# Kernel optimization log

Hardware: AMD Instinct MI355X
Metric: run time of the kernel (lower is better)

Reference implementation:

```python
import jax, jax.numpy as jnp
import numpy as np

B, L, C, V = 16, 600, 256, 256
OUT_SEQ = 6000
KSZ = 5
DILATIONS = (1, 2, 4)
N_BLOCKS = 10
COND = 256  # speaker(128) + noise(128)
TEMP = 10.0
EPS = 1e-5


def _ccbn(x, cond, gw, gb, bw, bb):
    # x: (B, C, L); conditional batch-norm: per-channel stats over (batch, length),
    # gamma/beta predicted from condition vector.
    mu = jnp.mean(x, axis=(0, 2), keepdims=True)
    var = jnp.var(x, axis=(0, 2), keepdims=True)
    xn = (x - mu) * jax.lax.rsqrt(var + EPS)
    gamma = 1.0 + cond @ gw + gb  # (B, C)
    beta = cond @ bw + bb         # (B, C)
    return xn * gamma[:, :, None] + beta[:, :, None]


def _conv1d(x, w, b, dil=1):
    # x: (B, C_in, L); w: (C_out, C_in, K)
    y = jax.lax.conv_general_dilated(
        x, w, window_strides=(1,), padding='SAME', rhs_dilation=(dil,),
        dimension_numbers=('NCH', 'OIH', 'NCH'))
    return y + b[None, :, None]


def setup_inputs() -> dict:
    key = jax.random.key(0)
    ks = jax.random.split(key, 20)
    s = 0.02
    inp = {
        'inputs': jax.random.randint(ks[0], (B, L), 0, V),
        'speaker_embeddings': jax.random.normal(ks[1], (B, 128), jnp.float32),
        'noise': jax.random.normal(ks[2], (B, 128), jnp.float32),
        'emb': jax.random.normal(ks[3], (V, C), jnp.float32) * s,
        # 10 blocks x 3 dilated convs
        'conv_w': jax.random.normal(ks[4], (N_BLOCKS, 3, C, C, KSZ), jnp.float32) * s,
        'conv_b': jnp.zeros((N_BLOCKS, 3, C), jnp.float32),
        # CCBN projections per conv (gamma/beta from condition)
        'g_w': jax.random.normal(ks[5], (N_BLOCKS, 3, COND, C), jnp.float32) * s,
        'g_b': jnp.zeros((N_BLOCKS, 3, C), jnp.float32),
        'b_w': jax.random.normal(ks[6], (N_BLOCKS, 3, COND, C), jnp.float32) * s,
        'b_b': jnp.zeros((N_BLOCKS, 3, C), jnp.float32),
        # TokenLength head: 2 CCBNs + conv1 (256->256,k1) + conv2 (256->1,k1)
        'tl_g_w': jax.random.normal(ks[7], (2, COND, C), jnp.float32) * s,
        'tl_g_b': jnp.zeros((2, C), jnp.float32),
        'tl_b_w': jax.random.normal(ks[8], (2, COND, C), jnp.float32) * s,
        'tl_b_b': jnp.zeros((2, C), jnp.float32),
        'tl_conv1_w': jax.random.normal(ks[9], (C, C, 1), jnp.float32) * s,
        'tl_conv1_b': jnp.zeros((C,), jnp.float32),
        'tl_conv2_w': jax.random.normal(ks[10], (1, C, 1), jnp.float32) * s,
        'tl_conv2_b': jnp.zeros((1,), jnp.float32),
    }
    return inp


def reference(inputs, speaker_embeddings, noise, emb, conv_w, conv_b,
              g_w, g_b, b_w, b_b, tl_g_w, tl_g_b, tl_b_w, tl_b_b,
              tl_conv1_w, tl_conv1_b, tl_conv2_w, tl_conv2_b):
    cond = jnp.concatenate([speaker_embeddings, noise], axis=-1)  # (B, COND)
    x = emb[inputs]                    # (B, L, C)
    x = jnp.transpose(x, (0, 2, 1))    # (B, C, L)

    # 10 unaligned blocks: residual stacks of CCBN -> ReLU -> dilated conv
    for blk in range(N_BLOCKS):
        y = x
        for j, d in enumerate(DILATIONS):
            y = jax.nn.relu(_ccbn(y, cond, g_w[blk, j], g_b[blk, j], b_w[blk, j], b_b[blk, j]))
            y = _conv1d(y, conv_w[blk, j], conv_b[blk, j], dil=d)
        x = x + y
    unaligned = x  # (B, C, L)

    # TokenLength head
    t = jax.nn.relu(_ccbn(unaligned, cond, tl_g_w[0], tl_g_b[0], tl_b_w[0], tl_b_b[0]))
    t = _conv1d(t, tl_conv1_w, tl_conv1_b)
    t = jax.nn.relu(_ccbn(t, cond, tl_g_w[1], tl_g_b[1], tl_b_w[1], tl_b_b[1]))
    t = _conv1d(t, tl_conv2_w, tl_conv2_b)  # (B, 1, L)
    token_lengths = jax.nn.relu(t[:, 0, :])  # (B, L)

    token_ends = jnp.cumsum(token_lengths, axis=-1)        # (B, L)
    token_centers = token_ends - token_lengths / 2.0        # (B, L)
    aligned_lengths = token_ends

    out_pos = jnp.arange(OUT_SEQ, dtype=jnp.float32)         # (OUT,)
    diff = token_centers[:, None, :] - out_pos[None, :, None]  # (B, OUT, L)
    logits = -(diff * diff) / TEMP
    weights = jax.nn.softmax(logits, axis=-1)                # (B, OUT, L)

    feats = jnp.transpose(unaligned, (0, 2, 1))              # (B, L, C)
    aligned_features = jnp.einsum('bol,blc->boc', weights, feats)  # (B, OUT, C)
    return aligned_features, aligned_lengths
```

## Files before the change

kernel.cpp:

```cpp
#include <hip/hip_runtime.h>
#include <math.h>
#include <stdint.h>

#define EPSv 1e-5f

typedef short short8 __attribute__((ext_vector_type(8)));
typedef float floatx4 __attribute__((ext_vector_type(4)));

__device__ __forceinline__ unsigned short f2bf(float x) {
  unsigned u = __float_as_uint(x);
  unsigned r = (u + 0x7fffu + ((u >> 16) & 1u)) >> 16;
  return (unsigned short)r;
}

__device__ __forceinline__ void gld_lds16(const void* g, void* l) {
  __builtin_amdgcn_global_load_lds(
      (const __attribute__((address_space(1))) unsigned*)(uintptr_t)g,
      (__attribute__((address_space(3))) unsigned*)(uintptr_t)l,
      16, 0, 0);
}

__global__ void k_zero(float* __restrict__ p) {
  p[blockIdx.x * 256 + threadIdx.x] = 0.f;
}

__global__ void k_gamma_beta(const float* __restrict__ spk, const float* __restrict__ noise,
                             const float* __restrict__ g_w, const float* __restrict__ g_b,
                             const float* __restrict__ b_w, const float* __restrict__ b_b,
                             const float* __restrict__ tl_g_w, const float* __restrict__ tl_g_b,
                             const float* __restrict__ tl_b_w, const float* __restrict__ tl_b_b,
                             float* __restrict__ gammas, float* __restrict__ betas) {
  __shared__ float condl[16*256];
  int t = threadIdx.x;
  for (int idx = t; idx < 4096; idx += 256) {
    int b = idx >> 8, k = idx & 255;
    condl[idx] = (k < 128) ? spk[b*128 + k] : noise[b*128 + k - 128];
  }
  __syncthreads();
  int i = blockIdx.x;
  const float *gw, *bw, *gbias, *bbias;
  if (i < 30) { gw = g_w + (size_t)i*65536; bw = b_w + (size_t)i*65536; gbias = g_b + i*256; bbias = b_b + i*256; }
  else { int j = i - 30; gw = tl_g_w + (size_t)j*65536; bw = tl_b_w + (size_t)j*65536; gbias = tl_g_b + j*256; bbias = tl_b_b + j*256; }
  int co = (t & 63) + blockIdx.y * 64;
  int slot = t >> 6;
  float g[4] = {0.f,0.f,0.f,0.f}, bt[4] = {0.f,0.f,0.f,0.f};
  for (int k = 0; k < 256; ++k) {
    float gwv = gw[k*256 + co];
    float bwv = bw[k*256 + co];
    #pragma unroll
    for (int bb = 0; bb < 4; ++bb) {
      float cv = condl[(slot*4 + bb)*256 + k];
      g[bb]  = fmaf(cv, gwv, g[bb]);
      bt[bb] = fmaf(cv, bwv, bt[bb]);
    }
  }
  #pragma unroll
  for (int bb = 0; bb < 4; ++bb) {
    int b = slot*4 + bb;
    gammas[i*4096 + b*256 + co] = 1.0f + g[bb] + gbias[co];
    betas [i*4096 + b*256 + co] = bt[bb] + bbias[co];
  }
}

template<int TAPS>
__device__ __forceinline__ void wprep_body(const float* __restrict__ src,
                                           unsigned short* __restrict__ dst,
                                           int cotile, int chunk, int t) {
  int cow = t >> 2, ci8 = (t & 3) * 8;
  const float* s0 = src + ((size_t)(cotile*64 + cow)*256 + chunk*32 + ci8)*TAPS;
  float v[8*TAPS];
  #pragma unroll
  for (int i = 0; i < 8*TAPS; ++i) v[i] = s0[i];
  unsigned short* dblk = dst + (size_t)cotile*(8*TAPS*4096) + (size_t)chunk*(TAPS*4096);
  #pragma unroll
  for (int tap = 0; tap < TAPS; ++tap) {
    unsigned hi2[4], lo2[4];
    #pragma unroll
    for (int jj = 0; jj < 4; ++jj) {
      float a = v[(jj*2+0)*TAPS + tap], b = v[(jj*2+1)*TAPS + tap];
      unsigned short ha = f2bf(a), hb = f2bf(b);
      unsigned short la = f2bf(a - __uint_as_float((unsigned)ha << 16));
      unsigned short lb = f2bf(b - __uint_as_float((unsigned)hb << 16));
      hi2[jj] = (unsigned)ha | ((unsigned)hb << 16);
      lo2[jj] = (unsigned)la | ((unsigned)lb << 16);
    }
    uint4 H; H.x = hi2[0]; H.y = hi2[1]; H.z = hi2[2]; H.w = hi2[3];
    uint4 L; L.x = lo2[0]; L.y = lo2[1]; L.z = lo2[2]; L.w = lo2[3];
    *(uint4*)(dblk + (size_t)(tap*2)*2048 + cow*32 + ci8) = H;
    *(uint4*)(dblk + (size_t)(tap*2+1)*2048 + cow*32 + ci8) = L;
  }
}

__global__ __launch_bounds__(256) void k_wprep(const float* __restrict__ conv_w,
                                               const float* __restrict__ tl_c1_w,
                                               unsigned short* __restrict__ wp) {
  int cc = blockIdx.x;
  int cotile = blockIdx.y >> 3, chunk = blockIdx.y & 7;
  if (cc == 30) wprep_body<1>(tl_c1_w, wp + (size_t)30*655360, cotile, chunk, threadIdx.x);
  else          wprep_body<5>(conv_w + (size_t)cc*327680, wp + (size_t)cc*655360, cotile, chunk, threadIdx.x);
}

__global__ void k_embed2(const int* __restrict__ inp, const float* __restrict__ emb,
                         float* __restrict__ x, float* __restrict__ stat0) {
  int bx = blockIdx.x;
  int c = threadIdx.x;
  int r0 = bx * 60;
  float s = 0.f, s2 = 0.f;
  for (int r = 0; r < 60; ++r) {
    int row = inp[r0 + r];
    float v = emb[(size_t)row*256 + c];
    x[(size_t)(r0 + r)*256 + c] = v;
    s += v; s2 = fmaf(v, v, s2);
  }
  atomicAdd(&stat0[c], s);
  atomicAdd(&stat0[256 + c], s2);
}

__global__ __launch_bounds__(256) void k_norm(const float* __restrict__ z,
                      const float* __restrict__ stat,
                      const float* __restrict__ gam, const float* __restrict__ bet,
                      unsigned short* __restrict__ zn) {
  __shared__ float s_sc[32];
  __shared__ float s_sh[32];
  int b = blockIdx.x, chunk = blockIdx.y, rg = blockIdx.z;
  int t = threadIdx.x;
  if (t < 32) {
    int c = chunk*32 + t;
    float s = stat[c], s2 = stat[256 + c];
    float mu = s * (1.0f/9600.0f);
    float var = s2 * (1.0f/9600.0f) - mu*mu;
    float rs = rsqrtf(var + EPSv);
    float scale = rs * gam[b*256 + c];
    s_sc[t] = scale;
    s_sh[t] = fmaf(-mu, scale, bet[b*256 + c]);
  }
  __syncthreads();
  int srow = t >> 3, fq = t & 7;
  float4 sc4 = *(const float4*)&s_sc[fq*4];
  float4 sh4 = *(const float4*)&s_sh[fq*4];
  unsigned short* zh = zn + ((size_t)b*8 + chunk)*54400 + fq*4;
  unsigned short* zl = zh + 27200;
  const float* zb = z + (size_t)b*600*256 + chunk*32 + fq*4;
  #pragma unroll
  for (int i = 0; i < 4; ++i) {
    int r = rg*128 + i*32 + srow;
    if (r < 680) {
      int l = r - 8;
      uint2 vh; vh.x = 0u; vh.y = 0u;
      uint2 vl; vl.x = 0u; vl.y = 0u;
      if (l >= 0 && l < 600) {
        float4 zv = *(const float4*)&zb[(size_t)l*256];
        float v0 = fmaxf(fmaf(zv.x, sc4.x, sh4.x), 0.f);
        float v1 = fmaxf(fmaf(zv.y, sc4.y, sh4.y), 0.f);
        float v2 = fmaxf(fmaf(zv.z, sc4.z, sh4.z), 0.f);
        float v3 = fmaxf(fmaf(zv.w, sc4.w, sh4.w), 0.f);
        unsigned short h0 = f2bf(v0), h1 = f2bf(v1), h2 = f2bf(v2), h3 = f2bf(v3);
        unsigned short e0 = f2bf(v0 - __uint_as_float((unsigned)h0 << 16));
        unsigned short e1 = f2bf(v1 - __uint_as_float((unsigned)h1 << 16));
        unsigned short e2 = f2bf(v2 - __uint_as_float((unsigned)h2 << 16));
        unsigned short e3 = f2bf(v3 - __uint_as_float((unsigned)h3 << 16));
        vh.x = (unsigned)h0 | ((unsigned)h1 << 16);
        vh.y = (unsigned)h2 | ((unsigned)h3 << 16);
        vl.x = (unsigned)e0 | ((unsigned)e1 << 16);
        vl.y = (unsigned)e2 | ((unsigned)e3 << 16);
      }
      *(uint2*)&zh[(size_t)r*40] = vh;
      *(uint2*)&zl[(size_t)r*40] = vl;
    }
  }
}

template<int TAPS>
__global__ __launch_bounds__(256) void k_convm(const unsigned short* __restrict__ zn,
                        float* __restrict__ out, float* __restrict__ stat_out,
                        const unsigned short* __restrict__ wpc,
                        const float* __restrict__ bias, int dil, int mode) {
  __shared__ __align__(16) unsigned short Zhi[2][3584];
  __shared__ __align__(16) unsigned short Zlo[2][3584];
  __shared__ float lsum[32];
  __shared__ float lsq[32];
  int t = threadIdx.x;
  int bx = blockIdx.x;
  int b  = bx / 10;
  int l0 = (bx % 10) * 64;
  int co0 = blockIdx.y * 32;
  int cobase = (blockIdx.y & 1) * 32;
  int PAD = ((TAPS - 1)/2) * dil;
  int w = t >> 6, lane = t & 63;
  int lsub = (w & 1) * 32, cosub = (w >> 1) * 16;
  int quad = lane >> 4, nlan = lane & 15;
  if (t < 32) { lsum[t] = 0.f; lsq[t] = 0.f; }

  floatx4 acc[2];
  acc[0] = (floatx4){0.f,0.f,0.f,0.f};
  acc[1] = (floatx4){0.f,0.f,0.f,0.f};

  const unsigned short* zbase = zn + (size_t)b*435200 + (size_t)(l0 - PAD + 8)*40 + (size_t)lane*8;
  int ar0 = (lsub + nlan) * 40 + quad * 8;
  int ar1 = ar0 + 640;

  #define STAGE(ch, bf) do {                                            \
    const unsigned short* srcp = zbase + (size_t)(ch)*54400;            \
    for (int i = w; i < 14; i += 4) {                                   \
      int p = (i >= 7) ? 1 : 0;                                         \
      int k = i - p*7;                                                  \
      gld_lds16(srcp + p*27200 + k*512, (p ? Zlo[bf] : Zhi[bf]) + k*512); \
    }                                                                   \
  } while (0)

  STAGE(0, 0);
  __syncthreads();

  for (int chunk = 0; chunk < 8; ++chunk) {
    int cb = chunk & 1;
    if (chunk < 7) STAGE(chunk + 1, cb ^ 1);
    const unsigned short* pch = wpc + (size_t)((blockIdx.y >> 1)*8 + chunk) * (TAPS*4096);
    short8 bh[TAPS], bl[TAPS];
    int cw = (cobase + cosub + nlan)*32 + quad*8;
    #pragma unroll
    for (int tap = 0; tap < TAPS; ++tap) {
      bh[tap] = *(const short8*)(pch + (size_t)(tap*2)*2048 + cw);
      bl[tap] = *(const short8*)(pch + (size_t)(tap*2+1)*2048 + cw);
    }
    #pragma unroll
    for (int tap = 0; tap < TAPS; ++tap) {
      int sh = tap * dil * 40;
      short8 ah0 = *(const short8*)&Zhi[cb][ar0 + sh];
      short8 ah1 = *(const short8*)&Zhi[cb][ar1 + sh];
      short8 al0 = *(const short8*)&Zlo[cb][ar0 + sh];
      short8 al1 = *(const short8*)&Zlo[cb][ar1 + sh];
      acc[0] = __builtin_amdgcn_mfma_f32_16x16x32_bf16(ah0, bh[tap], acc[0], 0, 0, 0);
      acc[0] = __builtin_amdgcn_mfma_f32_16x16x32_bf16(ah0, bl[tap], acc[0], 0, 0, 0);
      acc[0] = __builtin_amdgcn_mfma_f32_16x16x32_bf16(al0, bh[tap], acc[0], 0, 0, 0);
      acc[1] = __builtin_amdgcn_mfma_f32_16x16x32_bf16(ah1, bh[tap], acc[1], 0, 0, 0);
      acc[1] = __builtin_amdgcn_mfma_f32_16x16x32_bf16(ah1, bl[tap], acc[1], 0, 0, 0);
      acc[1] = __builtin_amdgcn_mfma_f32_16x16x32_bf16(al1, bh[tap], acc[1], 0, 0, 0);
    }
    __syncthreads();
  }
  #undef STAGE

  float bsv = bias[co0 + cosub + nlan];
  float ssum = 0.f, ssq = 0.f;
  #pragma unroll
  for (int mt = 0; mt < 2; ++mt) {
    #pragma unroll
    for (int r = 0; r < 4; ++r) {
      int l = l0 + lsub + mt*16 + quad*4 + r;
      if (l < 600) {
        float v = acc[mt][r] + bsv;
        float* dst = &out[((size_t)(b*600 + l))*256 + co0 + cosub + nlan];
        if (mode) v += *dst;
        *dst = v;
        ssum += v;
        ssq = fmaf(v, v, ssq);
      }
    }
  }
  ssum += __shfl_xor(ssum, 16, 64);
  ssum += __shfl_xor(ssum, 32, 64);
  ssq  += __shfl_xor(ssq, 16, 64);
  ssq  += __shfl_xor(ssq, 32, 64);
  if (quad == 0) {
    atomicAdd(&lsum[cosub + nlan], ssum);
    atomicAdd(&lsq [cosub + nlan], ssq);
  }
  __syncthreads();
  if (t < 32) {
    atomicAdd(&stat_out[co0 + t], lsum[t]);
    atomicAdd(&stat_out[256 + co0 + t], lsq[t]);
  }
}

__global__ void k_tl2(const float* __restrict__ z, const float* __restrict__ stat,
                      const float* __restrict__ gam, const float* __restrict__ bet,
                      const float* __restrict__ w2, const float* __restrict__ b2,
                      float* __restrict__ tl) {
  int t = threadIdx.x;
  int row = blockIdx.x * 4 + (t >> 6);
  int lane = t & 63;
  int b = row / 600;
  float4 s1 = *(const float4*)&stat[lane*4];
  float4 s2 = *(const float4*)&stat[256 + lane*4];
  float4 gm = *(const float4*)&gam[b*256 + lane*4];
  float4 bt = *(const float4*)&bet[b*256 + lane*4];
  float sc[4], sh[4];
  {
    float sv[4] = {s1.x, s1.y, s1.z, s1.w};
    float qv[4] = {s2.x, s2.y, s2.z, s2.w};
    float gv[4] = {gm.x, gm.y, gm.z, gm.w};
    float bv[4] = {bt.x, bt.y, bt.z, bt.w};
    #pragma unroll
    for (int i = 0; i < 4; ++i) {
      float mu = sv[i] * (1.0f/9600.0f);
      float var = qv[i] * (1.0f/9600.0f) - mu*mu;
      float rs = rsqrtf(var + EPSv);
      sc[i] = rs * gv[i];
      sh[i] = fmaf(-mu, sc[i], bv[i]);
    }
  }
  float4 zr = *(const float4*)&z[(size_t)row*256 + lane*4];
  float4 wr = *(const float4*)&w2[lane*4];
  float z0 = fmaxf(fmaf(zr.x, sc[0], sh[0]), 0.f);
  float z1 = fmaxf(fmaf(zr.y, sc[1], sh[1]), 0.f);
  float z2 = fmaxf(fmaf(zr.z, sc[2], sh[2]), 0.f);
  float z3 = fmaxf(fmaf(zr.w, sc[3], sh[3]), 0.f);
  float s = z0*wr.x + z1*wr.y + z2*wr.z + z3*wr.w;
  for (int m = 32; m >= 1; m >>= 1) s += __shfl_xor(s, m, 64);
  if (lane == 0) tl[row] = fmaxf(s + b2[0], 0.f);
}

__global__ void k_cumsum(const float* __restrict__ tl, float* __restrict__ centers,
                         float* __restrict__ out_len) {
  int b = blockIdx.x; int lane = threadIdx.x;
  float carry = 0.f;
  for (int ch = 0; ch < 10; ++ch) {
    int l = ch*64 + lane;
    float v = (l < 600) ? tl[b*600 + l] : 0.f;
    float s = v;
    #pragma unroll
    for (int off = 1; off < 64; off <<= 1) {
      float n = __shfl_up(s, off, 64);
      if (lane >= off) s += n;
    }
    float ends = carry + s;
    if (l < 600) {
      centers[b*600 + l] = ends - 0.5f*v;
      out_len[b*600 + l] = ends;
    }
    carry = __shfl(ends, 63, 64);
  }
}

__global__ void k_tobf16(const float* __restrict__ x, unsigned short* __restrict__ fbT) {
  __shared__ unsigned short T[64*66];
  int b = blockIdx.x, lt = blockIdx.y, ct = blockIdx.z;
  int t = threadIdx.x;
  int i4 = t >> 6;
  int j = t & 63;
  #pragma unroll
  for (int r = 0; r < 16; ++r) {
    int li = i4*16 + r;
    int l = lt*64 + li;
    float v = (l < 600) ? x[((size_t)(b*600 + l))*256 + ct*64 + j] : 0.f;
    T[j*66 + li] = f2bf(v);
  }
  __syncthreads();
  int row = t >> 2, seg = (t & 3) * 16;
  unsigned vv[8];
  #pragma unroll
  for (int k = 0; k < 8; ++k)
    vv[k] = *(const unsigned*)&T[row*66 + seg + k*2];
  size_t dsth = ((size_t)(b*256 + ct*64 + row))*640 + lt*64 + seg;
  unsigned* du = (unsigned*)fbT;
  uint4 a; a.x = vv[0]; a.y = vv[1]; a.z = vv[2]; a.w = vv[3];
  uint4 c4; c4.x = vv[4]; c4.y = vv[5]; c4.z = vv[6]; c4.w = vv[7];
  *(uint4*)(du + dsth/2) = a;
  *(uint4*)(du + dsth/2 + 4) = c4;
}

__global__ __launch_bounds__(256) void k_align2(const unsigned short* __restrict__ fbT,
                        const float* __restrict__ centers, float* __restrict__ outp) {
  __shared__ float cen[600];
  __shared__ float mrow[64];
  __shared__ float isum[64];
  __shared__ unsigned short Wt[64*72];
  __shared__ unsigned short Ft[256*72];
  int b = blockIdx.x;
  int o0 = blockIdx.y * 64;
  int t = threadIdx.x;
  int wv = t >> 6, lane = t & 63;
  for (int i = t; i < 600; i += 256) cen[i] = centers[b*600 + i];
  __syncthreads();
  for (int rr = 0; rr < 16; ++rr) {
    int oi = wv*16 + rr;
    float opos = (float)(o0 + oi);
    float mx = -3.0e38f;
    for (int l = lane; l < 600; l += 64) {
      float d = cen[l] - opos;
      mx = fmaxf(mx, -d*d*0.1f);
    }
    #pragma unroll
    for (int mm = 32; mm >= 1; mm >>= 1) mx = fmaxf(mx, __shfl_xor(mx, mm, 64));
    if (lane == 0) mrow[oi] = mx;
  }
  __syncthreads();
  floatx4 acc[4][4];
  #pragma unroll
  for (int i = 0; i < 4; ++i)
    #pragma unroll
    for (int j = 0; j < 4; ++j)
      acc[i][j] = (floatx4){0.f, 0.f, 0.f, 0.f};
  int quad = lane >> 4;
  int nlan = lane & 15;
  int oi_w = t >> 2;
  int sbase = t & 3;
  float mo = mrow[oi_w];
  float opos_w = (float)(o0 + oi_w);
  float psum = 0.f;
  const unsigned short* srcb = fbT + ((size_t)b*256)*640;

  for (int ch = 0; ch < 10; ++ch) {
    int lc0 = ch * 64;
    __syncthreads();
    #pragma unroll
    for (int sidx = 0; sidx < 2; ++sidx) {
      int seg = sbase + sidx*4;
      unsigned pk[4];
      #pragma unroll
      for (int jj = 0; jj < 8; jj += 2) {
        int li = lc0 + seg*8 + jj;
        float e0 = 0.f, e1 = 0.f;
        if (li < 600)     { float d = cen[li] - opos_w;     e0 = __expf(-d*d*0.1f - mo); }
        if (li + 1 < 600) { float d = cen[li + 1] - opos_w; e1 = __expf(-d*d*0.1f - mo); }
        psum += e0 + e1;
        pk[jj>>1] = (unsigned)f2bf(e0) | ((unsigned)f2bf(e1) << 16);
      }
      uint4 v; v.x = pk[0]; v.y = pk[1]; v.z = pk[2]; v.w = pk[3];
      *(uint4*)&Wt[oi_w*72 + seg*8] = v;
    }
    #pragma unroll
    for (int it = 0; it < 8; ++it) {
      int idx = t + it*256;
      int c = idx >> 3, part = idx & 7;
      uint4 v = *(const uint4*)(srcb + (size_t)c*640 + lc0 + part*8);
      *(uint4*)&Ft[c*72 + part*8] = v;
    }
    __syncthreads();
    #pragma unroll
    for (int ks = 0; ks < 2; ++ks) {
      int ko = ks*32 + quad*8;
      short8 af[4], bfr[4];
      #pragma unroll
      for (int mt = 0; mt < 4; ++mt)
        af[mt] = *(const short8*)&Wt[(mt*16 + nlan)*72 + ko];
      #pragma unroll
      for (int nt = 0; nt < 4; ++nt)
        bfr[nt] = *(const short8*)&Ft[(wv*64 + nt*16 + nlan)*72 + ko];
      #pragma unroll
      for (int mt = 0; mt < 4; ++mt)
        #pragma unroll
        for (int nt = 0; nt < 4; ++nt)
          acc[mt][nt] = __builtin_amdgcn_mfma_f32_16x16x32_bf16(af[mt], bfr[nt], acc[mt][nt], 0, 0, 0);
    }
  }
  psum += __shfl_xor(psum, 1, 64);
  psum += __shfl_xor(psum, 2, 64);
  if ((t & 3) == 0) isum[oi_w] = 1.0f / psum;
  __syncthreads();
  #pragma unroll
  for (int mt = 0; mt < 4; ++mt) {
    #pragma unroll
    for (int r = 0; r < 4; ++r) {
      int oi = mt*16 + quad*4 + r;
      int o = o0 + oi;
      if (o < 6000) {
        float sc = isum[oi];
        #pragma unroll
        for (int nt = 0; nt < 4; ++nt) {
          int c = wv*64 + nt*16 + nlan;
          outp[((size_t)b*6000 + o)*256 + c] = acc[mt][nt][r] * sc;
        }
      }
    }
  }
}

extern "C" void kernel_launch(void* const* d_in, const int* in_sizes, int n_in,
                              void* d_out, int out_size, void* d_ws, size_t ws_size,
                              hipStream_t stream) {
  const int*   inputs = (const int*)  d_in[0];
  const float* spk    = (const float*)d_in[1];
  const float* noise  = (const float*)d_in[2];
  const float* emb    = (const float*)d_in[3];
  const float* conv_w = (const float*)d_in[4];
  const float* conv_b = (const float*)d_in[5];
  const float* g_w    = (const float*)d_in[6];
  const float* g_b    = (const float*)d_in[7];
  const float* b_w    = (const float*)d_in[8];
  const float* b_b    = (const float*)d_in[9];
  const float* tl_g_w = (const float*)d_in[10];
  const float* tl_g_b = (const float*)d_in[11];
  const float* tl_b_w = (const float*)d_in[12];
  const float* tl_b_b = (const float*)d_in[13];
  const float* tl_c1_w = (const float*)d_in[14];
  const float* tl_c1_b = (const float*)d_in[15];
  const float* tl_c2_w = (const float*)d_in[16];
  const float* tl_c2_b = (const float*)d_in[17];
  float* out = (float*)d_out;

  float* ws = (float*)d_ws;
  float* x       = ws;
  float* A       = x + 2457600;
  float* Bf      = A + 2457600;
  float* gammas  = Bf + 2457600;
  float* betas   = gammas + 131072;
  float* statacc = betas + 131072;
  float* tl      = statacc + 16384;
  float* cen     = tl + 9600;
  unsigned short* wp = (unsigned short*)(cen + 9600);
  unsigned short* Zn = wp + (size_t)31*655360;
  unsigned short* fbT = (unsigned short*)Bf;

  k_zero<<<dim3(64), dim3(256), 0, stream>>>(statacc);
  k_wprep<<<dim3(31, 32), dim3(256), 0, stream>>>(conv_w, tl_c1_w, wp);
  k_gamma_beta<<<dim3(32, 4), dim3(256), 0, stream>>>(spk, noise, g_w, g_b, b_w, b_b,
      tl_g_w, tl_g_b, tl_b_w, tl_b_b, gammas, betas);
  k_embed2<<<dim3(160), dim3(256), 0, stream>>>(inputs, emb, x, statacc);

  const int dils[3] = {1, 2, 4};
  for (int blk = 0; blk < 10; ++blk) {
    const float* srcs[3] = {x, A, Bf};
    float*       dsts[3] = {A, Bf, x};
    for (int j = 0; j < 3; ++j) {
      int idx = blk*3 + j;
      int mode = (j == 2) ? 1 : 0;
      k_norm<<<dim3(16, 8, 6), dim3(256), 0, stream>>>(srcs[j],
          statacc + idx*512, gammas + idx*4096, betas + idx*4096, Zn);
      k_convm<5><<<dim3(160, 8), dim3(256), 0, stream>>>(Zn, dsts[j],
          statacc + (idx+1)*512,
          wp + (size_t)idx*655360, conv_b + idx*256, dils[j], mode);
    }
  }
  k_norm<<<dim3(16, 8, 6), dim3(256), 0, stream>>>(x,
      statacc + 30*512, gammas + 30*4096, betas + 30*4096, Zn);
  k_convm<1><<<dim3(160, 8), dim3(256), 0, stream>>>(Zn, A,
      statacc + 31*512,
      wp + (size_t)30*655360, tl_c1_b, 1, 0);
  k_tl2<<<dim3(2400), dim3(256), 0, stream>>>(A, statacc + 31*512,
      gammas + 31*4096, betas + 31*4096, tl_c2_w, tl_c2_b, tl);
  k_cumsum<<<dim3(16), dim3(64), 0, stream>>>(tl, cen, out + 24576000);
  k_tobf16<<<dim3(16, 10, 4), dim3(256), 0, stream>>>(x, fbT);
  k_align2<<<dim3(16, 94), dim3(256), 0, stream>>>(fbT, cen, out);
}
```

Before: 1.670 ms.

## Replace stat atomics with per-block partials and double-buffer align weights

```diff
diff --git a/kernel.cpp b/kernel.cpp
--- a/kernel.cpp
+++ b/kernel.cpp
@@ -18,10 +18,6 @@
       (const __attribute__((address_space(1))) unsigned*)(uintptr_t)g,
       (__attribute__((address_space(3))) unsigned*)(uintptr_t)l,
       16, 0, 0);
-}
-
-__global__ void k_zero(float* __restrict__ p) {
-  p[blockIdx.x * 256 + threadIdx.x] = 0.f;
 }
 
 __global__ void k_gamma_beta(const float* __restrict__ spk, const float* __restrict__ noise,
@@ -101,7 +97,7 @@
 }
 
 __global__ void k_embed2(const int* __restrict__ inp, const float* __restrict__ emb,
-                         float* __restrict__ x, float* __restrict__ stat0) {
+                         float* __restrict__ x, float* __restrict__ statp) {
   int bx = blockIdx.x;
   int c = threadIdx.x;
   int r0 = bx * 60;
@@ -112,21 +108,35 @@
     x[(size_t)(r0 + r)*256 + c] = v;
     s += v; s2 = fmaf(v, v, s2);
   }
-  atomicAdd(&stat0[c], s);
-  atomicAdd(&stat0[256 + c], s2);
+  statp[(size_t)bx*512 + c] = s;
+  statp[(size_t)bx*512 + 256 + c] = s2;
 }
 
 __global__ __launch_bounds__(256) void k_norm(const float* __restrict__ z,
-                      const float* __restrict__ stat,
+                      const float* __restrict__ statp,
                       const float* __restrict__ gam, const float* __restrict__ bet,
                       unsigned short* __restrict__ zn) {
   __shared__ float s_sc[32];
   __shared__ float s_sh[32];
+  __shared__ float red[2][32][8];
   int b = blockIdx.x, chunk = blockIdx.y, rg = blockIdx.z;
   int t = threadIdx.x;
+  {
+    int ch = t >> 3, g = t & 7;
+    int c = chunk*32 + ch;
+    float s = 0.f, s2 = 0.f;
+    for (int p = g; p < 160; p += 8) {
+      s  += statp[(size_t)p*512 + c];
+      s2 += statp[(size_t)p*512 + 256 + c];
+    }
+    red[0][ch][g] = s; red[1][ch][g] = s2;
+  }
+  __syncthreads();
   if (t < 32) {
+    float s = 0.f, s2 = 0.f;
+    #pragma unroll
+    for (int g = 0; g < 8; ++g) { s += red[0][t][g]; s2 += red[1][t][g]; }
     int c = chunk*32 + t;
-    float s = stat[c], s2 = stat[256 + c];
     float mu = s * (1.0f/9600.0f);
     float var = s2 * (1.0f/9600.0f) - mu*mu;
     float rs = rsqrtf(var + EPSv);
@@ -172,7 +182,7 @@
 
 template<int TAPS>
 __global__ __launch_bounds__(256) void k_convm(const unsigned short* __restrict__ zn,
-                        float* __restrict__ out, float* __restrict__ stat_out,
+                        float* __restrict__ out, float* __restrict__ statp,
                         const unsigned short* __restrict__ wpc,
                         const float* __restrict__ bias, int dil, int mode) {
   __shared__ __align__(16) unsigned short Zhi[2][3584];
@@ -267,9 +277,16 @@
   }
   __syncthreads();
   if (t < 32) {
-    atomicAdd(&stat_out[co0 + t], lsum[t]);
-    atomicAdd(&stat_out[256 + co0 + t], lsq[t]);
-  }
+    statp[(size_t)bx*512 + co0 + t] = lsum[t];
+    statp[(size_t)bx*512 + 256 + co0 + t] = lsq[t];
+  }
+}
+
+__global__ void k_statred(const float* __restrict__ sp, float* __restrict__ dst) {
+  int idx = blockIdx.x*256 + threadIdx.x;
+  float s = 0.f;
+  for (int p = 0; p < 160; ++p) s += sp[(size_t)p*512 + idx];
+  dst[idx] = s;
 }
 
 __global__ void k_tl2(const float* __restrict__ z, const float* __restrict__ stat,
@@ -359,13 +376,12 @@
   *(uint4*)(du + dsth/2 + 4) = c4;
 }
 
-__global__ __launch_bounds__(256) void k_align2(const unsigned short* __restrict__ fbT,
+__global__ __launch_bounds__(256, 4) void k_align2(const unsigned short* __restrict__ fbT,
                         const float* __restrict__ centers, float* __restrict__ outp) {
   __shared__ float cen[600];
   __shared__ float mrow[64];
   __shared__ float isum[64];
-  __shared__ unsigned short Wt[64*72];
-  __shared__ unsigned short Ft[256*72];
+  __shared__ unsigned short Wt[2][64*72];
   int b = blockIdx.x;
   int o0 = blockIdx.y * 64;
   int t = threadIdx.x;
@@ -399,51 +415,58 @@
   float opos_w = (float)(o0 + oi_w);
   float psum = 0.f;
   const unsigned short* srcb = fbT + ((size_t)b*256)*640;
+  const unsigned short* fbl = srcb + (size_t)(wv*64 + nlan)*640 + quad*8;
+
+  #define STAGE_WT(CH, BF) do {                                              \
+    int lcs = (CH) * 64;                                                     \
+    _Pragma("unroll")                                                        \
+    for (int sidx = 0; sidx < 2; ++sidx) {                                   \
+      int seg = sbase + sidx*4;                                              \
+      unsigned pk[4];                                                        \
+      _Pragma("unroll")                                                      \
+      for (int jj = 0; jj < 8; jj += 2) {                                    \
+        int li = lcs + seg*8 + jj;                                           \
+        float e0 = 0.f, e1 = 0.f;                                            \
+        if (li < 600)     { float d = cen[li] - opos_w;     e0 = __expf(-d*d*0.1f - mo); } \
+        if (li + 1 < 600) { float d = cen[li + 1] - opos_w; e1 = __expf(-d*d*0.1f - mo); } \
+        psum += e0 + e1;                                                     \
+        pk[jj>>1] = (unsigned)f2bf(e0) | ((unsigned)f2bf(e1) << 16);         \
+      }                                                                      \
+      uint4 v; v.x = pk[0]; v.y = pk[1]; v.z = pk[2]; v.w = pk[3];           \
+      *(uint4*)&Wt[BF][oi_w*72 + seg*8] = v;                                 \
+    }                                                                        \
+  } while (0)
+
+  STAGE_WT(0, 0);
+  __syncthreads();
 
   for (int ch = 0; ch < 10; ++ch) {
+    int rb = ch & 1;
     int lc0 = ch * 64;
-    __syncthreads();
-    #pragma unroll
-    for (int sidx = 0; sidx < 2; ++sidx) {
-      int seg = sbase + sidx*4;
-      unsigned pk[4];
+    short8 bfr[2][4];
+    #pragma unroll
+    for (int ks = 0; ks < 2; ++ks)
       #pragma unroll
-      for (int jj = 0; jj < 8; jj += 2) {
-        int li = lc0 + seg*8 + jj;
-        float e0 = 0.f, e1 = 0.f;
-        if (li < 600)     { float d = cen[li] - opos_w;     e0 = __expf(-d*d*0.1f - mo); }
-        if (li + 1 < 600) { float d = cen[li + 1] - opos_w; e1 = __expf(-d*d*0.1f - mo); }
-        psum += e0 + e1;
-        pk[jj>>1] = (unsigned)f2bf(e0) | ((unsigned)f2bf(e1) << 16);
-      }
-      uint4 v; v.x = pk[0]; v.y = pk[1]; v.z = pk[2]; v.w = pk[3];
-      *(uint4*)&Wt[oi_w*72 + seg*8] = v;
-    }
-    #pragma unroll
-    for (int it = 0; it < 8; ++it) {
-      int idx = t + it*256;
-      int c = idx >> 3, part = idx & 7;
-      uint4 v = *(const uint4*)(srcb + (size_t)c*640 + lc0 + part*8);
-      *(uint4*)&Ft[c*72 + part*8] = v;
-    }
-    __syncthreads();
+      for (int nt = 0; nt < 4; ++nt)
+        bfr[ks][nt] = *(const short8*)(fbl + (size_t)nt*16*640 + lc0 + ks*32);
+    if (ch < 9) STAGE_WT(ch + 1, rb ^ 1);
     #pragma unroll
     for (int ks = 0; ks < 2; ++ks) {
       int ko = ks*32 + quad*8;
-      short8 af[4], bfr[4];
+      short8 af[4];
       #pragma unroll
       for (int mt = 0; mt < 4; ++mt)
-        af[mt] = *(const short8*)&Wt[(mt*16 + nlan)*72 + ko];
-      #pragma unroll
-      for (int nt = 0; nt < 4; ++nt)
-        bfr[nt] = *(const short8*)&Ft[(wv*64 + nt*16 + nlan)*72 + ko];
+        af[mt] = *(const short8*)&Wt[rb][(mt*16 + nlan)*72 + ko];
       #pragma unroll
       for (int mt = 0; mt < 4; ++mt)
         #pragma unroll
         for (int nt = 0; nt < 4; ++nt)
-          acc[mt][nt] = __builtin_amdgcn_mfma_f32_16x16x32_bf16(af[mt], bfr[nt], acc[mt][nt], 0, 0, 0);
-    }
-  }
+          acc[mt][nt] = __builtin_amdgcn_mfma_f32_16x16x32_bf16(af[mt], bfr[ks][nt], acc[mt][nt], 0, 0, 0);
+    }
+    __syncthreads();
+  }
+  #undef STAGE_WT
+
   psum += __shfl_xor(psum, 1, 64);
   psum += __shfl_xor(psum, 2, 64);
   if ((t & 3) == 0) isum[oi_w] = 1.0f / psum;
@@ -495,18 +518,18 @@
   float* Bf      = A + 2457600;
   float* gammas  = Bf + 2457600;
   float* betas   = gammas + 131072;
-  float* statacc = betas + 131072;
-  float* tl      = statacc + 16384;
+  float* statp   = betas + 131072;
+  float* stat31  = statp + 81920;
+  float* tl      = stat31 + 512;
   float* cen     = tl + 9600;
   unsigned short* wp = (unsigned short*)(cen + 9600);
   unsigned short* Zn = wp + (size_t)31*655360;
   unsigned short* fbT = (unsigned short*)Bf;
 
-  k_zero<<<dim3(64), dim3(256), 0, stream>>>(statacc);
   k_wprep<<<dim3(31, 32), dim3(256), 0, stream>>>(conv_w, tl_c1_w, wp);
   k_gamma_beta<<<dim3(32, 4), dim3(256), 0, stream>>>(spk, noise, g_w, g_b, b_w, b_b,
       tl_g_w, tl_g_b, tl_b_w, tl_b_b, gammas, betas);
-  k_embed2<<<dim3(160), dim3(256), 0, stream>>>(inputs, emb, x, statacc);
+  k_embed2<<<dim3(160), dim3(256), 0, stream>>>(inputs, emb, x, statp);
 
   const int dils[3] = {1, 2, 4};
   for (int blk = 0; blk < 10; ++blk) {
@@ -516,18 +539,17 @@
       int idx = blk*3 + j;
       int mode = (j == 2) ? 1 : 0;
       k_norm<<<dim3(16, 8, 6), dim3(256), 0, stream>>>(srcs[j],
-          statacc + idx*512, gammas + idx*4096, betas + idx*4096, Zn);
+          statp, gammas + idx*4096, betas + idx*4096, Zn);
       k_convm<5><<<dim3(160, 8), dim3(256), 0, stream>>>(Zn, dsts[j],
-          statacc + (idx+1)*512,
-          wp + (size_t)idx*655360, conv_b + idx*256, dils[j], mode);
+          statp, wp + (size_t)idx*655360, conv_b + idx*256, dils[j], mode);
     }
   }
   k_norm<<<dim3(16, 8, 6), dim3(256), 0, stream>>>(x,
-      statacc + 30*512, gammas + 30*4096, betas + 30*4096, Zn);
+      statp, gammas + 30*4096, betas + 30*4096, Zn);
   k_convm<1><<<dim3(160, 8), dim3(256), 0, stream>>>(Zn, A,
-      statacc + 31*512,
-      wp + (size_t)30*655360, tl_c1_b, 1, 0);
-  k_tl2<<<dim3(2400), dim3(256), 0, stream>>>(A, statacc + 31*512,
+      statp, wp + (size_t)30*655360, tl_c1_b, 1, 0);
+  k_statred<<<dim3(2), dim3(256), 0, stream>>>(statp, stat31);
+  k_tl2<<<dim3(2400), dim3(256), 0, stream>>>(A, stat31,
       gammas + 31*4096, betas + 31*4096, tl_c2_w, tl_c2_b, tl);
   k_cumsum<<<dim3(16), dim3(64), 0, stream>>>(tl, cen, out + 24576000);
   k_tobf16<<<dim3(16, 10, 4), dim3(256), 0, stream>>>(x, fbT);
```

Measured after the change: 1.760 ms. +5.4%, slower.
